# Kernel tuning notes

Measured on AMD Instinct MI355X. Metric: run time of the kernel, lower is better.

## Reference

```python
import jax, jax.numpy as jnp
import numpy as np

B, N, C_IN, C_OUT, H = 8, 1024, 256, 512, 8
DH = C_OUT // H  # per-head dim
LN_EPS = 1e-5


def setup_inputs() -> dict:
    key = jax.random.key(0)
    ks = jax.random.split(key, 8)
    # xavier_normal std for [in, out] fan pair
    std = float(np.sqrt(2.0 / (C_IN + DH)))
    x = jax.random.normal(ks[0], (B, N, C_IN), dtype=jnp.float32)
    adj = jax.random.uniform(ks[1], (B, N, N), dtype=jnp.float32)
    W_q = jax.random.normal(ks[2], (H, C_IN, DH), dtype=jnp.float32) * std
    W_k = jax.random.normal(ks[3], (H, C_IN, DH), dtype=jnp.float32) * std
    W_v = jax.random.normal(ks[4], (H, C_IN, DH), dtype=jnp.float32) * std
    # Conv1d(in, out, kernel=1) == pointwise linear: weight [out, in], bias [out]
    bound = float(1.0 / np.sqrt(C_IN))
    conv_w = jax.random.uniform(ks[5], (C_OUT, C_IN), dtype=jnp.float32, minval=-bound, maxval=bound)
    conv_b = jax.random.uniform(ks[6], (C_OUT,), dtype=jnp.float32, minval=-bound, maxval=bound)
    ln_w = jnp.ones((C_OUT,), dtype=jnp.float32)
    ln_b = jnp.zeros((C_OUT,), dtype=jnp.float32)
    return {"x": x, "adj": adj, "W_q": W_q, "W_k": W_k, "W_v": W_v,
            "conv_w": conv_w, "conv_b": conv_b, "ln_w": ln_w, "ln_b": ln_b}


def reference(x, adj, W_q, W_k, W_v, conv_w, conv_b, ln_w, ln_b):
    # NOTE: in the original module, adj is used only to compute D_neg/A_hat,
    # which are discarded; it has no effect on the output. Attention is dense.
    dh = W_q.shape[-1]
    scale = 1.0 / jnp.sqrt(jnp.asarray(dh, dtype=x.dtype))
    # batched per-head projections: [B,N,Cin] x [H,Cin,dh] -> [B,H,N,dh]
    Q = jnp.einsum('bni,hio->bhno', x, W_q)
    K = jnp.einsum('bni,hio->bhno', x, W_k)
    V = jnp.einsum('bni,hio->bhno', x, W_v)
    scores = jnp.einsum('bhqd,bhkd->bhqk', Q, K) * scale  # [B,H,N,N]
    attn = jax.nn.softmax(scores, axis=-1)
    out = jax.nn.relu(jnp.einsum('bhqk,bhkd->bhqd', attn, V))  # [B,H,N,dh]
    b, h, n, d = out.shape
    out = out.transpose(0, 2, 1, 3).reshape(b, n, h * d)  # concat heads -> [B,N,Cout]
    # matching_conv: 1x1 conv == linear over channels
    proj = jnp.einsum('bni,oi->bno', x, conv_w) + conv_b
    y = out + proj
    mean = jnp.mean(y, axis=-1, keepdims=True)
    var = jnp.var(y, axis=-1, keepdims=True)
    y = (y - mean) * jax.lax.rsqrt(var + LN_EPS)
    return y * ln_w + ln_b
```

## Files before the change

kernel.cpp:

```cpp
#include <hip/hip_runtime.h>

#define B_ 8
#define N_ 1024
#define CIN_ 256
#define COUT_ 512
#define H_ 8
#define DH_ 64

typedef __attribute__((ext_vector_type(8))) short bf8;
typedef __attribute__((ext_vector_type(4))) short s4;
typedef __attribute__((ext_vector_type(4))) float f4;
typedef __attribute__((ext_vector_type(2))) unsigned int u2;

__device__ __forceinline__ short f2bf(float f) {
  unsigned u = __builtin_bit_cast(unsigned, f);
  u += 0x7fffu + ((u >> 16) & 1u);
  return (short)(u >> 16);
}
__device__ __forceinline__ float bf2f(short s) {
  unsigned u = ((unsigned)(unsigned short)s) << 16;
  return __builtin_bit_cast(float, u);
}

#if __has_builtin(__builtin_amdgcn_exp2f)
#define EXP2 __builtin_amdgcn_exp2f
#else
#define EXP2 exp2f
#endif

__device__ __forceinline__ unsigned cvtpk(float a, float b) {
  unsigned u;
  asm("v_cvt_pk_bf16_f32 %0, %1, %2" : "=v"(u) : "v"(a), "v"(b));
  return u;
}

#define MFMA16(a, b, c) __builtin_amdgcn_mfma_f32_16x16x32_bf16((a), (b), (c), 0, 0, 0)
#define MFMAPV(a, b, c) __builtin_amdgcn_mfma_f32_16x16x16bf16_1k((a), (b), (c), 0, 0, 0)

#define GLD16(gp, lp)                                                              \
  __builtin_amdgcn_global_load_lds((const __attribute__((address_space(1))) void*)(gp), \
                                   (__attribute__((address_space(3))) void*)(lp), 16, 0, 0)

__global__ void k_prep(const float* __restrict__ Wq, const float* __restrict__ Wk,
                       const float* __restrict__ Wv, const float* __restrict__ Cw,
                       const float* __restrict__ x, short* __restrict__ Wt,
                       short* __restrict__ xb) {
  int blk = blockIdx.x;
  if (blk < 2048) {
    int col = blk;
    int k = threadIdx.x;
    float v;
    if (col < 512) {
      int h = col >> 6, d = col & 63;
      v = Wq[(h * CIN_ + k) * DH_ + d];
    } else if (col < 1024) {
      int c = col - 512, h = c >> 6, d = c & 63;
      v = Wk[(h * CIN_ + k) * DH_ + d];
    } else if (col < 1536) {
      int c = col - 1024, h = c >> 6, d = c & 63;
      v = Wv[(h * CIN_ + k) * DH_ + d];
    } else {
      v = Cw[(col - 1536) * CIN_ + k];
    }
    Wt[col * CIN_ + k] = f2bf(v);
  } else {
    int i = (blk - 2048) * 256 + threadIdx.x;
    f4 a = *reinterpret_cast<const f4*>(x + (size_t)i * 8);
    f4 b = *reinterpret_cast<const f4*>(x + (size_t)i * 8 + 4);
    bf8 o;
    o[0] = f2bf(a[0]); o[1] = f2bf(a[1]); o[2] = f2bf(a[2]); o[3] = f2bf(a[3]);
    o[4] = f2bf(b[0]); o[5] = f2bf(b[1]); o[6] = f2bf(b[2]); o[7] = f2bf(b[3]);
    *reinterpret_cast<bf8*>(xb + (size_t)i * 8) = o;
  }
}

__global__ __launch_bounds__(256) void k_gemm(const short* __restrict__ xb, const short* __restrict__ Wt,
                                              short* __restrict__ Qt, short* __restrict__ Kw,
                                              short* __restrict__ Vt, short* __restrict__ Pj) {
  __shared__ short Al[2][128][64];
  __shared__ short Bl[2][128][64];
  int tid = threadIdx.x;
  int mt = blockIdx.x >> 4, nt = blockIdx.x & 15;
  int row0 = mt * 128, col0 = nt * 128;
  int w = tid >> 6, lane = tid & 63, g = lane >> 4, lr = lane & 15;
  int wm = w >> 1, wn = w & 1;
  f4 acc[4][4];
#pragma unroll
  for (int i = 0; i < 4; ++i)
#pragma unroll
    for (int j = 0; j < 4; ++j) acc[i][j] = (f4){0.f, 0.f, 0.f, 0.f};

  int srow[4], sgc[4];
#pragma unroll
  for (int p = 0; p < 4; ++p) {
    int s = p * 256 + tid;
    srow[p] = s >> 3;
    sgc[p] = (s & 7) ^ (srow[p] & 7);
  }

#define STAGE_AB(k0_, buf_)                                                     \
  {                                                                             \
    char* abase = (char*)&Al[buf_][0][0];                                       \
    char* bbase = (char*)&Bl[buf_][0][0];                                       \
    _Pragma("unroll")                                                           \
    for (int p = 0; p < 4; ++p) {                                               \
      int lb = (p * 256 + w * 64) << 4;                                         \
      GLD16(xb + (row0 + srow[p]) * CIN_ + (k0_) + sgc[p] * 8, abase + lb);     \
      GLD16(Wt + (col0 + srow[p]) * CIN_ + (k0_) + sgc[p] * 8, bbase + lb);     \
    }                                                                           \
  }

  STAGE_AB(0, 0);

  for (int kt = 0; kt < 4; ++kt) {
    int cur = kt & 1;
    if (kt < 3) {
      STAGE_AB((kt + 1) * 64, cur ^ 1);
      asm volatile("s_waitcnt vmcnt(8)" ::: "memory");
    } else {
      asm volatile("s_waitcnt vmcnt(0)" ::: "memory");
    }
    __builtin_amdgcn_s_barrier();

    const short* al = &Al[cur][0][0];
    const short* bl = &Bl[cur][0][0];
    bf8 af[4][2], bb[4][2];
#pragma unroll
    for (int mi = 0; mi < 4; ++mi) {
      int R = wm * 64 + mi * 16 + lr;
      int sw = R & 7;
      af[mi][0] = *reinterpret_cast<const bf8*>(al + R * 64 + ((g ^ sw) * 8));
      af[mi][1] = *reinterpret_cast<const bf8*>(al + R * 64 + (((4 + g) ^ sw) * 8));
    }
#pragma unroll
    for (int ni = 0; ni < 4; ++ni) {
      int R = wn * 64 + ni * 16 + lr;
      int sw = R & 7;
      bb[ni][0] = *reinterpret_cast<const bf8*>(bl + R * 64 + ((g ^ sw) * 8));
      bb[ni][1] = *reinterpret_cast<const bf8*>(bl + R * 64 + (((4 + g) ^ sw) * 8));
    }
#pragma unroll
    for (int mi = 0; mi < 4; ++mi)
#pragma unroll
      for (int ni = 0; ni < 4; ++ni) {
        acc[mi][ni] = MFMA16(af[mi][0], bb[ni][0], acc[mi][ni]);
        acc[mi][ni] = MFMA16(af[mi][1], bb[ni][1], acc[mi][ni]);
      }
    asm volatile("s_waitcnt lgkmcnt(0)" ::: "memory");
    __builtin_amdgcn_s_barrier();
  }

  const float QSCL = 0.125f * 1.4426950408889634f;
#pragma unroll
  for (int mi = 0; mi < 4; ++mi)
#pragma unroll
    for (int ni = 0; ni < 4; ++ni) {
      int c = col0 + wn * 64 + ni * 16 + lr;
      int r0 = row0 + wm * 64 + mi * 16 + g * 4;
      int b = r0 >> 10, n0 = r0 & 1023;
      if (c < 512) {
        int hh = c >> 6, d = c & 63;
        s4 vv;
#pragma unroll
        for (int j = 0; j < 4; ++j) vv[j] = f2bf(acc[mi][ni][j] * QSCL);
        *reinterpret_cast<s4*>(Qt + ((size_t)(b * H_ + hh) * DH_ + d) * N_ + n0) = vv;
      } else if (c < 1024) {
        int cc = c - 512;
#pragma unroll
        for (int j = 0; j < 4; ++j) {
          int n = n0 + j;
          Kw[((b * H_ + (cc >> 6)) * N_ + n) * DH_ + (cc & 63)] = f2bf(acc[mi][ni][j]);
        }
      } else if (c < 1536) {
        int cc = c - 1024;
        int hh = cc >> 6, d = cc & 63;
        s4 vv;
#pragma unroll
        for (int j = 0; j < 4; ++j) vv[j] = f2bf(acc[mi][ni][j]);
        *reinterpret_cast<s4*>(Vt + ((size_t)(b * H_ + hh) * DH_ + d) * N_ + n0) = vv;
      } else {
#pragma unroll
        for (int j = 0; j < 4; ++j) {
          Pj[(size_t)(r0 + j) * COUT_ + (c - 1536)] = f2bf(acc[mi][ni][j]);
        }
      }
    }
}

__global__ __launch_bounds__(256) void k_attn(const short* __restrict__ Qt, const short* __restrict__ Kw,
                                              const short* __restrict__ Vt, const short* __restrict__ Pj,
                                              short* __restrict__ At) {
  __shared__ short Kl[4][64][64];
  __shared__ short Vl[4][64][64];
  int tid = threadIdx.x;
  int nid = ((blockIdx.x & 7) << 6) | (blockIdx.x >> 3);
  int bh = nid >> 3;
  int qb = nid & 7;
  int w = tid >> 6, lane = tid & 63, g = lane >> 4, lr = lane & 15;
  int qglob = qb * 128 + w * 32;
  const short* Qp = Qt + (size_t)bh * DH_ * N_;
  const short* Kp = Kw + (size_t)bh * N_ * DH_;
  const short* Vp = Vt + (size_t)bh * DH_ * N_;

  bf8 aq[2][2];
#pragma unroll
  for (int qs = 0; qs < 2; ++qs) {
    int n = qglob + qs * 16 + lr;
#pragma unroll
    for (int e = 0; e < 8; ++e) {
      aq[qs][0][e] = Qp[(size_t)(g * 8 + e) * N_ + n];
      aq[qs][1][e] = Qp[(size_t)(32 + g * 8 + e) * N_ + n];
    }
  }

  int sr0 = tid >> 3, sc0 = (tid & 7) ^ (sr0 & 7);
  int s1 = tid + 256;
  int sr1 = s1 >> 3, sc1 = (s1 & 7) ^ (sr1 & 7);
  int lo0 = (w * 64) << 4;
  int lo1 = (w * 64 + 256) << 4;

#define STAGE_KV(tt_, buf_)                                                     \
  {                                                                             \
    const short* kb = Kp + (tt_) * (64 * DH_);                                  \
    const short* vb = Vp + (tt_) * 64;                                          \
    char* klb = (char*)&Kl[buf_][0][0];                                         \
    char* vlb = (char*)&Vl[buf_][0][0];                                         \
    GLD16(kb + sr0 * 64 + sc0 * 8, klb + lo0);                                  \
    GLD16(kb + sr1 * 64 + sc1 * 8, klb + lo1);                                  \
    GLD16(vb + (size_t)sr0 * N_ + sc0 * 8, vlb + lo0);                          \
    GLD16(vb + (size_t)sr1 * N_ + sc1 * 8, vlb + lo1);                          \
  }

  STAGE_KV(0, 0);
  STAGE_KV(1, 1);

  f4 o[2][4];
  f4 lacc[2];
#pragma unroll
  for (int qs = 0; qs < 2; ++qs) {
    lacc[qs] = (f4){0.f, 0.f, 0.f, 0.f};
#pragma unroll
    for (int i = 0; i < 4; ++i) o[qs][i] = (f4){0.f, 0.f, 0.f, 0.f};
  }

  for (int t = 0; t < 16; ++t) {
    int cur = t & 3;
    if (t < 14) {
      STAGE_KV(t + 2, (t + 2) & 3);
      asm volatile("s_waitcnt vmcnt(8)" ::: "memory");
    } else if (t == 14) {
      asm volatile("s_waitcnt vmcnt(4)" ::: "memory");
    } else {
      asm volatile("s_waitcnt vmcnt(0)" ::: "memory");
    }
    __builtin_amdgcn_s_barrier();

    const short* klc = &Kl[cur][0][0];
    bf8 bk0[4], bk1[4];
#pragma unroll
    for (int kt = 0; kt < 4; ++kt) {
      int R = kt * 16 + lr;
      const short* kr = klc + R * 64;
      int sw = (R & 7) << 3;
      bk0[kt] = *reinterpret_cast<const bf8*>(kr + ((g * 8) ^ sw));
      bk1[kt] = *reinterpret_cast<const bf8*>(kr + ((32 + g * 8) ^ sw));
    }
    f4 s0[4], s1v[4];
    __builtin_amdgcn_s_setprio(1);
#pragma unroll
    for (int kt = 0; kt < 4; ++kt) {
      f4 z = (f4){0.f, 0.f, 0.f, 0.f};
      z = MFMA16(bk0[kt], aq[0][0], z);
      z = MFMA16(bk1[kt], aq[0][1], z);
      s0[kt] = z;
      f4 z2 = (f4){0.f, 0.f, 0.f, 0.f};
      z2 = MFMA16(bk0[kt], aq[1][0], z2);
      z2 = MFMA16(bk1[kt], aq[1][1], z2);
      s1v[kt] = z2;
    }
    __builtin_amdgcn_s_setprio(0);
    s4 pq0[4], pq1[4];
#pragma unroll
    for (int kt = 0; kt < 4; ++kt) {
      f4 p;
      p[0] = EXP2(s0[kt][0]); p[1] = EXP2(s0[kt][1]);
      p[2] = EXP2(s0[kt][2]); p[3] = EXP2(s0[kt][3]);
      lacc[0] += p;
      u2 pk;
      pk[0] = cvtpk(p[0], p[1]);
      pk[1] = cvtpk(p[2], p[3]);
      pq0[kt] = __builtin_bit_cast(s4, pk);
    }
#pragma unroll
    for (int kt = 0; kt < 4; ++kt) {
      f4 p;
      p[0] = EXP2(s1v[kt][0]); p[1] = EXP2(s1v[kt][1]);
      p[2] = EXP2(s1v[kt][2]); p[3] = EXP2(s1v[kt][3]);
      lacc[1] += p;
      u2 pk;
      pk[0] = cvtpk(p[0], p[1]);
      pk[1] = cvtpk(p[2], p[3]);
      pq1[kt] = __builtin_bit_cast(s4, pk);
    }

    const short* vlc = &Vl[cur][0][0];
#pragma unroll
    for (int dt = 0; dt < 4; ++dt) {
      int R = dt * 16 + lr;
      const short* vr = vlc + R * 64;
      int swR = R & 7;
      s4 va[4];
#pragma unroll
      for (int kt = 0; kt < 4; ++kt) {
        int ch = (kt * 2 + (g >> 1)) ^ swR;
        va[kt] = *reinterpret_cast<const s4*>(vr + ch * 8 + (g & 1) * 4);
      }
      __builtin_amdgcn_s_setprio(1);
#pragma unroll
      for (int kt = 0; kt < 4; ++kt) {
        o[0][dt] = MFMAPV(va[kt], pq0[kt], o[0][dt]);
        o[1][dt] = MFMAPV(va[kt], pq1[kt], o[1][dt]);
      }
      __builtin_amdgcn_s_setprio(0);
    }
    asm volatile("s_waitcnt lgkmcnt(0)" ::: "memory");
  }

  float ls[2];
#pragma unroll
  for (int qs = 0; qs < 2; ++qs) {
    float v = (lacc[qs][0] + lacc[qs][1]) + (lacc[qs][2] + lacc[qs][3]);
    v += __shfl_xor(v, 16, 64);
    v += __shfl_xor(v, 32, 64);
    ls[qs] = v;
  }
  int b = bh >> 3, h = bh & 7;
#pragma unroll
  for (int qs = 0; qs < 2; ++qs) {
    float inv = 1.f / ls[qs];
    int n = qglob + qs * 16 + lr;
    const short* pr = Pj + ((size_t)b * N_ + n) * COUT_ + h * DH_;
    short* dst = At + ((size_t)b * N_ + n) * COUT_ + h * DH_;
#pragma unroll
    for (int dt = 0; dt < 4; ++dt) {
      s4 pj4 = *reinterpret_cast<const s4*>(pr + dt * 16 + g * 4);
      s4 ov;
#pragma unroll
      for (int j = 0; j < 4; ++j)
        ov[j] = f2bf(fmaxf(o[qs][dt][j] * inv, 0.f) + bf2f(pj4[j]));
      *reinterpret_cast<s4*>(dst + dt * 16 + g * 4) = ov;
    }
  }
}

__global__ __launch_bounds__(256) void k_ln(const short* __restrict__ At,
                                            const float* __restrict__ cb, const float* __restrict__ lw,
                                            const float* __restrict__ lb, float* __restrict__ out) {
  int row = blockIdx.x * 4 + (threadIdx.x >> 6);
  int lane = threadIdx.x & 63;
  int c0 = lane * 8;
  bf8 a8 = *reinterpret_cast<const bf8*>(At + (size_t)row * COUT_ + c0);
  float y[8];
  float sum = 0.f, sq = 0.f;
#pragma unroll
  for (int j = 0; j < 8; ++j) {
    float v = bf2f(a8[j]) + cb[c0 + j];
    y[j] = v;
    sum += v;
    sq += v * v;
  }
#pragma unroll
  for (int off = 1; off < 64; off <<= 1) {
    sum += __shfl_xor(sum, off, 64);
    sq += __shfl_xor(sq, off, 64);
  }
  float mean = sum * (1.f / 512.f);
  float var = sq * (1.f / 512.f) - mean * mean;
  float rstd = rsqrtf(var + 1e-5f);
  f4 o0, o1;
#pragma unroll
  for (int j = 0; j < 4; ++j) o0[j] = (y[j] - mean) * rstd * lw[c0 + j] + lb[c0 + j];
#pragma unroll
  for (int j = 0; j < 4; ++j) o1[j] = (y[4 + j] - mean) * rstd * lw[c0 + 4 + j] + lb[c0 + 4 + j];
  *reinterpret_cast<f4*>(out + (size_t)row * COUT_ + c0) = o0;
  *reinterpret_cast<f4*>(out + (size_t)row * COUT_ + c0 + 4) = o1;
}

extern "C" void kernel_launch(void* const* d_in, const int* in_sizes, int n_in,
                              void* d_out, int out_size, void* d_ws, size_t ws_size,
                              hipStream_t stream) {
  const float* x  = (const float*)d_in[0];
  const float* Wq = (const float*)d_in[2];
  const float* Wk = (const float*)d_in[3];
  const float* Wv = (const float*)d_in[4];
  const float* Cw = (const float*)d_in[5];
  const float* cb = (const float*)d_in[6];
  const float* lw = (const float*)d_in[7];
  const float* lb = (const float*)d_in[8];
  float* out = (float*)d_out;
  char* ws = (char*)d_ws;
  short* xb = (short*)(ws);
  short* Wt = (short*)(ws + (size_t)4194304);
  short* Qt = (short*)(ws + (size_t)5242880);
  short* Kw = (short*)(ws + (size_t)13631488);
  short* Vt = (short*)(ws + (size_t)22020096);
  short* Pj = (short*)(ws + (size_t)30408704);
  short* At = (short*)(ws + (size_t)38797312);

  hipLaunchKernelGGL(k_prep, dim3(3072), dim3(256), 0, stream, Wq, Wk, Wv, Cw, x, Wt, xb);
  hipLaunchKernelGGL(k_gemm, dim3(1024), dim3(256), 0, stream, xb, Wt, Qt, Kw, Vt, Pj);
  hipLaunchKernelGGL(k_attn, dim3(512), dim3(256), 0, stream, Qt, Kw, Vt, Pj, At);
  hipLaunchKernelGGL(k_ln, dim3(2048), dim3(256), 0, stream, At, cb, lw, lb, out);
}
```

Baseline: 65.94 us.

## Use 128-key KV tiles with double buffering in attention loop

The attention kernel now stages K/V in 128-key tiles with two buffers instead of 64-key tiles with four buffers. That halves the number of loop iterations and barriers, and each iteration processes two 64-key halves. A second barrier per iteration is added to protect buffer reuse, because the prefetch distance drops from two tiles to one. The V shared-memory swizzle changes to a 16-chunk XOR pattern to fit the wider rows. The intent is to cut per-tile sync and loop overhead, but the shallower prefetch may expose more load latency.

New measurement: 66.31 us. About the same (+0.5%).

```diff
diff --git a/kernel.cpp b/kernel.cpp
--- a/kernel.cpp
+++ b/kernel.cpp
@@ -190,8 +190,8 @@
 __global__ __launch_bounds__(256) void k_attn(const short* __restrict__ Qt, const short* __restrict__ Kw,
                                               const short* __restrict__ Vt, const short* __restrict__ Pj,
                                               short* __restrict__ At) {
-  __shared__ short Kl[4][64][64];
-  __shared__ short Vl[4][64][64];
+  __shared__ short Kl[2][128][64];
+  __shared__ short Vl[2][64][128];
   int tid = threadIdx.x;
   int nid = ((blockIdx.x & 7) << 6) | (blockIdx.x >> 3);
   int bh = nid >> 3;
@@ -213,26 +213,31 @@
     }
   }
 
-  int sr0 = tid >> 3, sc0 = (tid & 7) ^ (sr0 & 7);
-  int s1 = tid + 256;
-  int sr1 = s1 >> 3, sc1 = (s1 & 7) ^ (sr1 & 7);
-  int lo0 = (w * 64) << 4;
-  int lo1 = (w * 64 + 256) << 4;
+  int krow[4], kgc[4], vrow[4], vgc[4];
+#pragma unroll
+  for (int p = 0; p < 4; ++p) {
+    int s = p * 256 + tid;
+    krow[p] = s >> 3;
+    kgc[p] = (s & 7) ^ (krow[p] & 7);
+    vrow[p] = s >> 4;
+    vgc[p] = (s & 15) ^ (vrow[p] & 15);
+  }
 
 #define STAGE_KV(tt_, buf_)                                                     \
   {                                                                             \
-    const short* kb = Kp + (tt_) * (64 * DH_);                                  \
-    const short* vb = Vp + (tt_) * 64;                                          \
+    const short* kb = Kp + (tt_) * (128 * DH_);                                 \
+    const short* vb = Vp + (tt_) * 128;                                         \
     char* klb = (char*)&Kl[buf_][0][0];                                         \
     char* vlb = (char*)&Vl[buf_][0][0];                                         \
-    GLD16(kb + sr0 * 64 + sc0 * 8, klb + lo0);                                  \
-    GLD16(kb + sr1 * 64 + sc1 * 8, klb + lo1);                                  \
-    GLD16(vb + (size_t)sr0 * N_ + sc0 * 8, vlb + lo0);                          \
-    GLD16(vb + (size_t)sr1 * N_ + sc1 * 8, vlb + lo1);                          \
+    _Pragma("unroll")                                                           \
+    for (int p = 0; p < 4; ++p) {                                               \
+      int lb = (p * 256 + w * 64) << 4;                                         \
+      GLD16(kb + krow[p] * DH_ + kgc[p] * 8, klb + lb);                         \
+      GLD16(vb + (size_t)vrow[p] * N_ + vgc[p] * 8, vlb + lb);                  \
+    }                                                                           \
   }
 
   STAGE_KV(0, 0);
-  STAGE_KV(1, 1);
 
   f4 o[2][4];
   f4 lacc[2];
@@ -243,87 +248,87 @@
     for (int i = 0; i < 4; ++i) o[qs][i] = (f4){0.f, 0.f, 0.f, 0.f};
   }
 
-  for (int t = 0; t < 16; ++t) {
-    int cur = t & 3;
-    if (t < 14) {
-      STAGE_KV(t + 2, (t + 2) & 3);
+  for (int t = 0; t < 8; ++t) {
+    int cur = t & 1;
+    if (t < 7) {
+      STAGE_KV(t + 1, cur ^ 1);
       asm volatile("s_waitcnt vmcnt(8)" ::: "memory");
-    } else if (t == 14) {
-      asm volatile("s_waitcnt vmcnt(4)" ::: "memory");
     } else {
       asm volatile("s_waitcnt vmcnt(0)" ::: "memory");
     }
     __builtin_amdgcn_s_barrier();
 
     const short* klc = &Kl[cur][0][0];
-    bf8 bk0[4], bk1[4];
-#pragma unroll
-    for (int kt = 0; kt < 4; ++kt) {
-      int R = kt * 16 + lr;
-      const short* kr = klc + R * 64;
-      int sw = (R & 7) << 3;
-      bk0[kt] = *reinterpret_cast<const bf8*>(kr + ((g * 8) ^ sw));
-      bk1[kt] = *reinterpret_cast<const bf8*>(kr + ((32 + g * 8) ^ sw));
-    }
-    f4 s0[4], s1v[4];
-    __builtin_amdgcn_s_setprio(1);
-#pragma unroll
-    for (int kt = 0; kt < 4; ++kt) {
-      f4 z = (f4){0.f, 0.f, 0.f, 0.f};
-      z = MFMA16(bk0[kt], aq[0][0], z);
-      z = MFMA16(bk1[kt], aq[0][1], z);
-      s0[kt] = z;
-      f4 z2 = (f4){0.f, 0.f, 0.f, 0.f};
-      z2 = MFMA16(bk0[kt], aq[1][0], z2);
-      z2 = MFMA16(bk1[kt], aq[1][1], z2);
-      s1v[kt] = z2;
-    }
-    __builtin_amdgcn_s_setprio(0);
-    s4 pq0[4], pq1[4];
-#pragma unroll
-    for (int kt = 0; kt < 4; ++kt) {
-      f4 p;
-      p[0] = EXP2(s0[kt][0]); p[1] = EXP2(s0[kt][1]);
-      p[2] = EXP2(s0[kt][2]); p[3] = EXP2(s0[kt][3]);
-      lacc[0] += p;
-      u2 pk;
-      pk[0] = cvtpk(p[0], p[1]);
-      pk[1] = cvtpk(p[2], p[3]);
-      pq0[kt] = __builtin_bit_cast(s4, pk);
-    }
-#pragma unroll
-    for (int kt = 0; kt < 4; ++kt) {
-      f4 p;
-      p[0] = EXP2(s1v[kt][0]); p[1] = EXP2(s1v[kt][1]);
-      p[2] = EXP2(s1v[kt][2]); p[3] = EXP2(s1v[kt][3]);
-      lacc[1] += p;
-      u2 pk;
-      pk[0] = cvtpk(p[0], p[1]);
-      pk[1] = cvtpk(p[2], p[3]);
-      pq1[kt] = __builtin_bit_cast(s4, pk);
-    }
-
     const short* vlc = &Vl[cur][0][0];
 #pragma unroll
-    for (int dt = 0; dt < 4; ++dt) {
-      int R = dt * 16 + lr;
-      const short* vr = vlc + R * 64;
-      int swR = R & 7;
-      s4 va[4];
+    for (int h2 = 0; h2 < 2; ++h2) {
+      bf8 bk0[4], bk1[4];
 #pragma unroll
       for (int kt = 0; kt < 4; ++kt) {
-        int ch = (kt * 2 + (g >> 1)) ^ swR;
-        va[kt] = *reinterpret_cast<const s4*>(vr + ch * 8 + (g & 1) * 4);
-      }
+        int R = h2 * 64 + kt * 16 + lr;
+        const short* kr = klc + R * 64;
+        int sw = (R & 7) << 3;
+        bk0[kt] = *reinterpret_cast<const bf8*>(kr + ((g * 8) ^ sw));
+        bk1[kt] = *reinterpret_cast<const bf8*>(kr + ((32 + g * 8) ^ sw));
+      }
+      f4 s0[4], s1v[4];
       __builtin_amdgcn_s_setprio(1);
 #pragma unroll
       for (int kt = 0; kt < 4; ++kt) {
-        o[0][dt] = MFMAPV(va[kt], pq0[kt], o[0][dt]);
-        o[1][dt] = MFMAPV(va[kt], pq1[kt], o[1][dt]);
+        f4 z = (f4){0.f, 0.f, 0.f, 0.f};
+        z = MFMA16(bk0[kt], aq[0][0], z);
+        z = MFMA16(bk1[kt], aq[0][1], z);
+        s0[kt] = z;
+        f4 z2 = (f4){0.f, 0.f, 0.f, 0.f};
+        z2 = MFMA16(bk0[kt], aq[1][0], z2);
+        z2 = MFMA16(bk1[kt], aq[1][1], z2);
+        s1v[kt] = z2;
       }
       __builtin_amdgcn_s_setprio(0);
+      s4 pq0[4], pq1[4];
+#pragma unroll
+      for (int kt = 0; kt < 4; ++kt) {
+        f4 p;
+        p[0] = EXP2(s0[kt][0]); p[1] = EXP2(s0[kt][1]);
+        p[2] = EXP2(s0[kt][2]); p[3] = EXP2(s0[kt][3]);
+        lacc[0] += p;
+        u2 pk;
+        pk[0] = cvtpk(p[0], p[1]);
+        pk[1] = cvtpk(p[2], p[3]);
+        pq0[kt] = __builtin_bit_cast(s4, pk);
+      }
+#pragma unroll
+      for (int kt = 0; kt < 4; ++kt) {
+        f4 p;
+        p[0] = EXP2(s1v[kt][0]); p[1] = EXP2(s1v[kt][1]);
+        p[2] = EXP2(s1v[kt][2]); p[3] = EXP2(s1v[kt][3]);
+        lacc[1] += p;
+        u2 pk;
+        pk[0] = cvtpk(p[0], p[1]);
+        pk[1] = cvtpk(p[2], p[3]);
+        pq1[kt] = __builtin_bit_cast(s4, pk);
+      }
+#pragma unroll
+      for (int dt = 0; dt < 4; ++dt) {
+        int Rv = dt * 16 + lr;
+        const short* vr = vlc + Rv * 128;
+        s4 va[4];
+#pragma unroll
+        for (int kt = 0; kt < 4; ++kt) {
+          int ch = (h2 * 8 + kt * 2 + (g >> 1)) ^ lr;
+          va[kt] = *reinterpret_cast<const s4*>(vr + ch * 8 + (g & 1) * 4);
+        }
+        __builtin_amdgcn_s_setprio(1);
+#pragma unroll
+        for (int kt = 0; kt < 4; ++kt) {
+          o[0][dt] = MFMAPV(va[kt], pq0[kt], o[0][dt]);
+          o[1][dt] = MFMAPV(va[kt], pq1[kt], o[1][dt]);
+        }
+        __builtin_amdgcn_s_setprio(0);
+      }
     }
     asm volatile("s_waitcnt lgkmcnt(0)" ::: "memory");
+    __builtin_amdgcn_s_barrier();
   }
 
   float ls[2];
```
